# Kernel tuning notes

Measured on AMD Instinct MI355X. Metric: run time of the kernel, lower is better.

The kernel has to match this reference:

```python
import jax, jax.numpy as jnp
import numpy as np

B, C, S = 256, 1024, 14   # batch, channels, spatial (frozen by y.view(b,c,14,14))
C2 = 15                   # channels2 in the module
CAT = C // 2 * 3 + C2     # 1551 = 15 + 512 + 1024
EPS = 1e-5


def _conv(x, w, b, groups, pad):
    out = jax.lax.conv_general_dilated(
        x, w, window_strides=(1, 1), padding=((pad, pad), (pad, pad)),
        dimension_numbers=('NCHW', 'OIHW', 'NCHW'), feature_group_count=groups)
    return out + b[None, :, None, None]


def _bn(x, gamma, beta):
    # training-mode BatchNorm2d: biased batch stats over (N,H,W)
    m = x.mean((0, 2, 3), keepdims=True)
    v = x.var((0, 2, 3), keepdims=True)
    return (x - m) * jax.lax.rsqrt(v + EPS) * gamma[None, :, None, None] + beta[None, :, None, None]


def setup_inputs() -> dict:
    key = jax.random.key(0)
    ks = jax.random.split(key, 16)
    r = C2 // 7  # = 2
    inp = {
        'y': jax.random.normal(ks[0], (B, C2, S * S), jnp.float32),
        'x': jax.random.normal(ks[1], (B, C, S, S), jnp.float32),
        'fc1_w': jax.random.normal(ks[2], (r, C2), jnp.float32) * 0.2,
        'fc2_w': jax.random.normal(ks[3], (C2, r), jnp.float32) * 0.2,
        'conv_w': jax.random.normal(ks[4], (C // 2, C, 1, 1), jnp.float32) * 0.03,
        'conv_b': jnp.zeros((C // 2,), jnp.float32),
        'dconv_w': jax.random.normal(ks[5], (C, 1, 3, 3), jnp.float32) * 0.2,
        'dconv_b': jnp.zeros((C,), jnp.float32),
        'dw1_w': jax.random.normal(ks[6], (CAT, 1, 3, 3), jnp.float32) * 0.2,
        'dw1_b': jnp.zeros((CAT,), jnp.float32),
        'pw1_w': jax.random.normal(ks[7], (C // 2, CAT, 1, 1), jnp.float32) * 0.03,
        'pw1_b': jnp.zeros((C // 2,), jnp.float32),
        'gamma': jnp.ones((C // 2,), jnp.float32),
        'beta': jnp.zeros((C // 2,), jnp.float32),
        'n': 0,
    }
    return inp


def reference(y, x, fc1_w, fc2_w, conv_w, conv_b, dconv_w, dconv_b,
              dw1_w, dw1_b, pw1_w, pw1_b, gamma, beta, n):
    b = y.shape[0]
    y4 = y.reshape(b, C2, S, S)
    # SE block on the 15 sub-channels
    g = y4.mean((2, 3))                              # (b, 15) global avg pool
    h = jax.nn.relu(g @ fc1_w.T) @ fc2_w.T           # (b, 15)
    y1 = y4 * jax.nn.sigmoid(h)[:, :, None, None]
    # depthwise conv on x, then per-(b,c) row covariance of the 14x14 map
    x1 = _conv(x, dconv_w, dconv_b, C, 1)            # (b, C, 14, 14)
    x2 = jax.lax.stop_gradient(x1)                   # .detach() in the original
    xc = x2 - x2.mean(-1, keepdims=True)             # np.cov: rows=vars, cols=obs
    cov = jnp.einsum('bcik,bcjk->bcij', xc, xc) / (S - 1)
    z = _conv(cov, conv_w, conv_b, 1, 0)             # 1x1 conv C -> C//2
    z = jax.nn.sigmoid(_bn(z, gamma, beta))
    for _ in range(n):                               # n=0 at these shapes
        y1 = jax.image.resize(y1, (y1.shape[0], y1.shape[1], y1.shape[2] * 2, y1.shape[3] * 2), 'bilinear')
    cat = jnp.concatenate([y1, z, x], axis=1)        # (b, 1551, 14, 14)
    o = _conv(cat, dw1_w, dw1_b, CAT, 1)             # depthwise 3x3
    o = _conv(o, pw1_w, pw1_b, 1, 0)                 # pointwise 1x1 -> C//2
    return jax.nn.relu(_bn(o, gamma, beta))
```

## Files before the change

### kernel.cpp

```cpp
#include <hip/hip_runtime.h>

typedef unsigned int u32;
typedef unsigned short u16;
typedef __attribute__((ext_vector_type(8))) short bf16x8;
typedef __attribute__((ext_vector_type(4))) float f32x4;
typedef __attribute__((ext_vector_type(4))) u32 u32x4;

#define EPSBN 1e-5f

#define GLDS16(gp, lp) __builtin_amdgcn_global_load_lds( \
    (const __attribute__((address_space(1))) u32*)(gp), \
    (__attribute__((address_space(3))) u32*)(lp), 16, 0, 0)

#define OFF_ADW    0ull
#define OFF_COVT   0ull
#define OFF_S      160563200ull
#define OFF_WBZ    160578560ull
#define OFF_WBP    161627136ull
#define OFF_STATSZ 163265536ull
#define OFF_STATSO 163269632ull
#define OFF_SCZ    163273728ull
#define OFF_SHZ    163275776ull
#define OFF_SCO    163277824ull
#define OFF_SHO    163279872ull

static __device__ __forceinline__ float bf2f(u16 h){
  u32 u = ((u32)h) << 16; float f; __builtin_memcpy(&f, &u, 4); return f;
}
static __device__ __forceinline__ u16 f2bf(float f){
  u32 u; __builtin_memcpy(&u, &f, 4);
  u = (u + 0x7fffu + ((u >> 16) & 1u)) >> 16;
  return (u16)u;
}

__global__ __launch_bounds__(64) void se_kernel(const float* __restrict__ y,
    const float* __restrict__ fc1, const float* __restrict__ fc2, float* __restrict__ sse){
  __shared__ float g[15];
  __shared__ float t[2];
  int b = blockIdx.x, l = threadIdx.x;
  for (int c = 0; c < 15; ++c){
    float p = 0.f;
    for (int k = l; k < 196; k += 64) p += y[((size_t)b*15 + c)*196 + k];
    p += __shfl_xor(p, 32); p += __shfl_xor(p, 16); p += __shfl_xor(p, 8);
    p += __shfl_xor(p, 4);  p += __shfl_xor(p, 2);  p += __shfl_xor(p, 1);
    if (l == 0) g[c] = p * (1.f/196.f);
  }
  __syncthreads();
  if (l < 2){
    float a = 0.f;
    for (int c = 0; c < 15; ++c) a += g[c] * fc1[l*15 + c];
    t[l] = fmaxf(a, 0.f);
  }
  __syncthreads();
  if (l < 15){
    float h = t[0]*fc2[l*2] + t[1]*fc2[l*2+1];
    sse[b*15 + l] = 1.f / (1.f + __expf(-h));
  }
}

__global__ void wconv_kernel(const float* __restrict__ cw, const float* __restrict__ pw,
                             u16* __restrict__ wbz, u16* __restrict__ wbp){
  u32 stride = gridDim.x * blockDim.x;
  for (u32 i = blockIdx.x*blockDim.x + threadIdx.x; i < 524288u; i += stride)
    wbz[i] = f2bf(cw[i]);
  for (u32 i = blockIdx.x*blockDim.x + threadIdx.x; i < 819200u; i += stride){
    u32 n = i / 1600u, k = i - n*1600u;
    wbp[i] = f2bf(k < 1551u ? pw[(size_t)n*1551 + k] : 0.f);
  }
}

__global__ __launch_bounds__(256,5) void cov_kernel(const float* __restrict__ x,
    const float* __restrict__ dcw, const float* __restrict__ dcb, u16* __restrict__ covT){
  __shared__ __align__(16) float xs[16*200];
  __shared__ __align__(16) u32 xcb[16*132];
  __shared__ float wls[16][9];
  __shared__ float wlb[16];
  u32* covL32 = (u32*)xs;

  int tid = threadIdx.x;
  int c0 = blockIdx.x * 16, b = blockIdx.y;

  {
    const float4* xg = (const float4*)(x + ((size_t)b*1024 + c0)*196);
    for (int i = tid; i < 784; i += 256){
      float4 v = xg[i];
      u32 c = (u32)i / 49u, p4 = (u32)i - c*49u;
      *(float4*)&xs[c*200u + p4*4u] = v;
    }
  }
  if (tid < 144) wls[tid/9][tid%9] = dcw[(size_t)(c0 + tid/9)*9 + (tid%9)];
  if (tid < 16) wlb[tid] = dcb[c0 + tid];
  __syncthreads();

  {
    int c = tid >> 4, i = tid & 15;
    u32 q[8];
    #pragma unroll
    for (int j = 0; j < 8; ++j) q[j] = 0u;
    if (i < 14){
      float wr[9];
      #pragma unroll
      for (int qq = 0; qq < 9; ++qq) wr[qq] = wls[c][qq];
      float topm = (i > 0) ? 1.f : 0.f, botm = (i < 13) ? 1.f : 0.f;
      wr[0] *= topm; wr[1] *= topm; wr[2] *= topm;
      wr[6] *= botm; wr[7] *= botm; wr[8] *= botm;
      float bb = wlb[c];
      float rr[3][16];
      #pragma unroll
      for (int d = 0; d < 3; ++d){
        rr[d][0] = 0.f; rr[d][15] = 0.f;
        int rowr = i + d - 1;
        rowr = rowr < 0 ? 0 : (rowr > 13 ? 13 : rowr);
        const float* src = &xs[c*200 + rowr*14];
        #pragma unroll
        for (int j = 0; j < 7; ++j)
          *(float2*)&rr[d][1 + 2*j] = *(const float2*)&src[2*j];
      }
      float ov[14];
      #pragma unroll
      for (int k = 0; k < 14; ++k){
        float a = bb;
        #pragma unroll
        for (int dy = 0; dy < 3; ++dy)
          #pragma unroll
          for (int dx = 0; dx < 3; ++dx)
            a += wr[dy*3+dx] * rr[dy][k + dx];
        ov[k] = a;
      }
      float mean = 0.f;
      #pragma unroll
      for (int k = 0; k < 14; ++k) mean += ov[k];
      mean *= (1.f/14.f);
      #pragma unroll
      for (int j = 0; j < 7; ++j){
        u32 lo = f2bf(ov[2*j]   - mean);
        u32 hi = f2bf(ov[2*j+1] - mean);
        q[j] = lo | (hi << 16);
      }
    }
    u32x4 q0 = {q[0], q[1], q[2], q[3]};
    u32x4 q1 = {q[4], q[5], q[6], q[7]};
    *(u32x4*)&xcb[c*132 + i*8]     = q0;
    *(u32x4*)&xcb[c*132 + i*8 + 4] = q1;
  }
  __syncthreads();

  {
    int w = tid >> 6, l = tid & 63, lr = l & 15, lq = l >> 4;
    #pragma unroll
    for (int pp = 0; pp < 2; ++pp){
      int clo = w*4 + 2*pp;
      bf16x8 alo = {0,0,0,0,0,0,0,0}, ahi = {0,0,0,0,0,0,0,0};
      if (lq < 2){
        alo = *(const bf16x8*)&xcb[clo*132 + lr*8 + lq*4];
        ahi = *(const bf16x8*)&xcb[(clo+1)*132 + lr*8 + lq*4];
      }
      f32x4 dlo = {0.f,0.f,0.f,0.f}, dhi = {0.f,0.f,0.f,0.f};
      dlo = __builtin_amdgcn_mfma_f32_16x16x32_bf16(alo, alo, dlo, 0, 0, 0);
      dhi = __builtin_amdgcn_mfma_f32_16x16x32_bf16(ahi, ahi, dhi, 0, 0, 0);
      if (lr < 14){
        int cp = w*2 + pp;
        #pragma unroll
        for (int r = 0; r < 4; ++r){
          int rowi = lq*4 + r;
          if (rowi < 14){
            u32 vv = (u32)f2bf(dlo[r] * (1.f/13.f)) | ((u32)f2bf(dhi[r] * (1.f/13.f)) << 16);
            covL32[cp*210 + rowi*14 + lr] = vv;
          }
        }
      }
    }
  }
  __syncthreads();

  for (int i = tid; i < 1568; i += 256){
    int cp = i & 7, ij = i >> 3;
    u32 v = covL32[cp*210 + ij];
    *(u32*)(covT + ((size_t)(b*196 + ij)*1024 + c0 + 2*cp)) = v;
  }
}

__global__ __launch_bounds__(256,5) void adw_kernel(
    const float* __restrict__ y, const float* __restrict__ sse,
    const u16* __restrict__ zT, const float* __restrict__ scz, const float* __restrict__ shz,
    const float* __restrict__ x, const float* __restrict__ dw1w, const float* __restrict__ dw1b,
    u16* __restrict__ Adw){
  __shared__ __align__(16) float ms[32*202];
  __shared__ float wd[32][9];
  __shared__ float bd[32];
  int tid = threadIdx.x;
  int cc0 = blockIdx.x * 32, b = blockIdx.y;

  for (int i = tid; i < 288; i += 256){
    int c = i / 9, q = i - c*9;
    int cc = cc0 + c;
    wd[c][q] = (cc < 1551) ? dw1w[(size_t)cc*9 + q] : 0.f;
  }
  if (tid < 32) bd[tid] = (cc0 + tid < 1551) ? dw1b[cc0 + tid] : 0.f;

  if (cc0 < 15){
    int ny = 15;
    for (int i = tid; i < ny*196; i += 256){
      u32 c = (u32)i / 196u, p = (u32)i - c*196u;
      ms[c*202u + p] = y[((size_t)b*15 + c)*196 + p] * sse[b*15 + c];
    }
  }
  {
    int zs = cc0 > 15 ? cc0 : 15;
    int ze = cc0 + 32 < 527 ? cc0 + 32 : 527;
    if (zs < ze){
      int nz = ze - zs, lbase = zs - cc0, obase = zs - 15;
      const u16* zrow = zT + (size_t)obase*50176 + (size_t)b*196;
      for (int i = tid; i < nz*98; i += 256){
        u32 oo = (u32)i / 98u, pp = (u32)i - oo*98u;
        u32 v = *(const u32*)(zrow + (size_t)oo*50176 + pp*2u);
        int o = obase + (int)oo;
        float s = scz[o], h = shz[o];
        float v0 = bf2f((u16)(v & 0xffffu)) * s + h;
        float v1 = bf2f((u16)(v >> 16))     * s + h;
        v0 = 1.f / (1.f + __expf(-v0));
        v1 = 1.f / (1.f + __expf(-v1));
        float2 fv = {v0, v1};
        *(float2*)&ms[(u32)(lbase + (int)oo)*202u + pp*2u] = fv;
      }
    }
  }
  {
    int xs_ = cc0 > 527 ? cc0 : 527;
    int xe = cc0 + 32 < 1551 ? cc0 + 32 : 1551;
    if (xs_ < xe){
      int nx = xe - xs_, lbase = xs_ - cc0, cxs = xs_ - 527;
      const float4* xg = (const float4*)(x + ((size_t)b*1024 + cxs)*196);
      for (int i = tid; i < nx*49; i += 256){
        float4 v = xg[i];
        u32 c = (u32)i / 49u, p4 = (u32)i - c*49u;
        float* dst = &ms[(u32)(lbase + (int)c)*202u + p4*4u];
        float2 lo = {v.x, v.y}, hi = {v.z, v.w};
        *(float2*)dst = lo;
        *(float2*)(dst + 2) = hi;
      }
    }
  }
  {
    int ps = cc0 > 1551 ? cc0 : 1551;
    int pe = cc0 + 32;
    if (ps < pe){
      int np = pe - ps, lbase = ps - cc0;
      for (int i = tid; i < np*196; i += 256){
        u32 c = (u32)i / 196u, p = (u32)i - c*196u;
        ms[(u32)(lbase + (int)c)*202u + p] = 0.f;
      }
    }
  }
  __syncthreads();

  for (int t = tid; t < 448; t += 256){
    int cc = t & 31, i = t >> 5;
    float wr[9];
    #pragma unroll
    for (int qq = 0; qq < 9; ++qq) wr[qq] = wd[cc][qq];
    float topm = (i > 0) ? 1.f : 0.f, botm = (i < 13) ? 1.f : 0.f;
    wr[0] *= topm; wr[1] *= topm; wr[2] *= topm;
    wr[6] *= botm; wr[7] *= botm; wr[8] *= botm;
    float bb = bd[cc];
    float rr[3][16];
    #pragma unroll
    for (int d = 0; d < 3; ++d){
      rr[d][0] = 0.f; rr[d][15] = 0.f;
      int rowr = i + d - 1;
      rowr = rowr < 0 ? 0 : (rowr > 13 ? 13 : rowr);
      const float* src = &ms[cc*202 + rowr*14];
      #pragma unroll
      for (int j = 0; j < 7; ++j)
        *(float2*)&rr[d][1 + 2*j] = *(const float2*)&src[2*j];
    }
    size_t obase = ((size_t)b*196 + i*14) * 1600 + cc0 + cc;
    #pragma unroll
    for (int k = 0; k < 14; ++k){
      float a = bb;
      #pragma unroll
      for (int dy = 0; dy < 3; ++dy)
        #pragma unroll
        for (int dx = 0; dx < 3; ++dx)
          a += wr[dy*3+dx] * rr[dy][k + dx];
      Adw[obase + (size_t)k*1600] = f2bf(a);
    }
  }
}

template<int MODE>
__global__ __launch_bounds__(256,3) void gemm_kernel(
    const u16* __restrict__ A, const u16* __restrict__ Bw,
    const float* __restrict__ bias, void* __restrict__ outp,
    float* __restrict__ stats, int K){
  __shared__ __align__(16) char smem[33280];
  u16* As = (u16*)smem;
  u16* Bs = (u16*)(smem + 16384);

  int tid = threadIdx.x;
  int w = tid >> 6, l = tid & 63;
  int wm = w >> 1, wn = w & 1;
  int lr = l & 15, lq = l >> 4;
  int m0 = blockIdx.y * 128;
  int n0 = blockIdx.x * 128;

  f32x4 acc[4][4] = {};
  int kTiles = K >> 6;

  for (int kt = 0; kt < kTiles; ++kt){
    if (kt) __syncthreads();
    #pragma unroll
    for (int i = 0; i < 4; ++i){
      int s = tid + i*256;
      int row = s >> 3, c8 = s & 7, sc = c8 ^ (row & 7);
      GLDS16(A  + (size_t)(m0 + row)*K + kt*64 + sc*8, As + s*8);
      GLDS16(Bw + (size_t)(n0 + row)*K + kt*64 + sc*8, Bs + s*8);
    }
    __syncthreads();
    #pragma unroll
    for (int ks = 0; ks < 2; ++ks){
      bf16x8 af[4], bfv[4];
      #pragma unroll
      for (int mi = 0; mi < 4; ++mi){
        int row = wm*64 + mi*16 + lr;
        int q = (ks*4 + lq) ^ (row & 7);
        af[mi] = *(const bf16x8*)(As + row*64 + q*8);
      }
      #pragma unroll
      for (int ni = 0; ni < 4; ++ni){
        int row = wn*64 + ni*16 + lr;
        int q = (ks*4 + lq) ^ (row & 7);
        bfv[ni] = *(const bf16x8*)(Bs + row*64 + q*8);
      }
      #pragma unroll
      for (int mi = 0; mi < 4; ++mi)
        #pragma unroll
        for (int ni = 0; ni < 4; ++ni)
          acc[mi][ni] = __builtin_amdgcn_mfma_f32_16x16x32_bf16(af[mi], bfv[ni], acc[mi][ni], 0, 0, 0);
    }
  }

  #pragma unroll
  for (int ni = 0; ni < 4; ++ni){
    int col = n0 + wn*64 + ni*16 + lr;
    float bb = bias[col];
    float s1 = 0.f, s2 = 0.f;
    #pragma unroll
    for (int mi = 0; mi < 4; ++mi)
      #pragma unroll
      for (int r = 0; r < 4; ++r){
        float v = acc[mi][ni][r] + bb;
        acc[mi][ni][r] = v;
        s1 += v; s2 += v*v;
      }
    s1 += __shfl_xor(s1, 16); s1 += __shfl_xor(s1, 32);
    s2 += __shfl_xor(s2, 16); s2 += __shfl_xor(s2, 32);
    if (lq == 0){
      atomicAdd(&stats[col], s1);
      atomicAdd(&stats[512 + col], s2);
    }
  }

  __syncthreads();
  float* eb = (float*)smem;
  #pragma unroll
  for (int rnd = 0; rnd < 2; ++rnd){
    if (wm == rnd){
      float* e = eb + wn * (64*65);
      #pragma unroll
      for (int mi = 0; mi < 4; ++mi)
        #pragma unroll
        for (int ni = 0; ni < 4; ++ni)
          #pragma unroll
          for (int r = 0; r < 4; ++r)
            e[(mi*16 + lq*4 + r)*65 + ni*16 + lr] = acc[mi][ni][r];
      int m = m0 + wm*64 + l;
      if (MODE == 0){
        u16* ob = (u16*)outp + (size_t)(n0 + wn*64)*50176 + m;
        #pragma unroll 8
        for (int no = 0; no < 64; ++no)
          ob[(size_t)no*50176] = f2bf(e[l*65 + no]);
      } else {
        u32 bq = (u32)m / 196u;
        u32 ij = (u32)m - bq*196u;
        float* ob = (float*)outp + ((size_t)bq*512 + n0 + wn*64)*196 + ij;
        #pragma unroll 8
        for (int no = 0; no < 64; ++no)
          ob[(size_t)no*196] = e[l*65 + no];
      }
    }
    __syncthreads();
  }
}

__global__ void bnprep_kernel(const float* __restrict__ stats, const float* __restrict__ gamma,
    const float* __restrict__ beta, float* __restrict__ sc, float* __restrict__ sh){
  int o = threadIdx.x;
  float m = stats[o] * (1.f/50176.f);
  float v = stats[512+o] * (1.f/50176.f) - m*m;
  float inv = rsqrtf(v + EPSBN);
  float g = gamma[o] * inv;
  sc[o] = g;
  sh[o] = beta[o] - m*g;
}

__global__ void final_kernel(float4* __restrict__ o4, const float* __restrict__ sc,
                             const float* __restrict__ sh){
  u32 stride = gridDim.x * blockDim.x;
  for (u32 i = blockIdx.x*blockDim.x + threadIdx.x; i < 6422528u; i += stride){
    u32 oc = (i / 49u) & 511u;
    float s = sc[oc], t = sh[oc];
    float4 v = o4[i];
    v.x = fmaxf(fmaf(v.x, s, t), 0.f);
    v.y = fmaxf(fmaf(v.y, s, t), 0.f);
    v.z = fmaxf(fmaf(v.z, s, t), 0.f);
    v.w = fmaxf(fmaf(v.w, s, t), 0.f);
    o4[i] = v;
  }
}

extern "C" void kernel_launch(void* const* d_in, const int* in_sizes, int n_in,
                              void* d_out, int out_size, void* d_ws, size_t ws_size,
                              hipStream_t stream){
  (void)in_sizes; (void)n_in; (void)out_size; (void)ws_size;
  const float* y      = (const float*)d_in[0];
  const float* x      = (const float*)d_in[1];
  const float* fc1    = (const float*)d_in[2];
  const float* fc2    = (const float*)d_in[3];
  const float* convw  = (const float*)d_in[4];
  const float* convb  = (const float*)d_in[5];
  const float* dconvw = (const float*)d_in[6];
  const float* dconvb = (const float*)d_in[7];
  const float* dw1w   = (const float*)d_in[8];
  const float* dw1b   = (const float*)d_in[9];
  const float* pw1w   = (const float*)d_in[10];
  const float* pw1b   = (const float*)d_in[11];
  const float* gamma  = (const float*)d_in[12];
  const float* beta   = (const float*)d_in[13];

  char* ws = (char*)d_ws;
  u16* covT   = (u16*)(ws + OFF_COVT);
  u16* Adw    = (u16*)(ws + OFF_ADW);
  float* sse  = (float*)(ws + OFF_S);
  u16* wbz    = (u16*)(ws + OFF_WBZ);
  u16* wbp    = (u16*)(ws + OFF_WBP);
  float* statsZ = (float*)(ws + OFF_STATSZ);
  float* statsO = (float*)(ws + OFF_STATSO);
  float* scz  = (float*)(ws + OFF_SCZ);
  float* shz  = (float*)(ws + OFF_SHZ);
  float* sco  = (float*)(ws + OFF_SCO);
  float* sho  = (float*)(ws + OFF_SHO);
  u16* zT     = (u16*)d_out;
  float* outf = (float*)d_out;

  hipMemsetAsync(statsZ, 0, 8192, stream);
  se_kernel<<<256, 64, 0, stream>>>(y, fc1, fc2, sse);
  wconv_kernel<<<2048, 256, 0, stream>>>(convw, pw1w, wbz, wbp);
  cov_kernel<<<dim3(64, 256), 256, 0, stream>>>(x, dconvw, dconvb, covT);
  gemm_kernel<0><<<dim3(4, 392), 256, 0, stream>>>(covT, wbz, convb, (void*)zT, statsZ, 1024);
  bnprep_kernel<<<1, 512, 0, stream>>>(statsZ, gamma, beta, scz, shz);
  adw_kernel<<<dim3(50, 256), 256, 0, stream>>>(y, sse, zT, scz, shz, x, dw1w, dw1b, Adw);
  gemm_kernel<1><<<dim3(4, 392), 256, 0, stream>>>(Adw, wbp, pw1b, (void*)outf, statsO, 1600);
  bnprep_kernel<<<1, 512, 0, stream>>>(statsO, gamma, beta, sco, sho);
  final_kernel<<<8192, 256, 0, stream>>>((float4*)outf, sco, sho);
}
```

Baseline: 524.3 us.

## Retile GEMMs so each 512-thread block covers all 512 output columns

Both pointwise GEMMs now run one 512-thread block per 64-row M tile, and that block computes all 512 N columns across 8 waves. The large activation matrix A is therefore read from global memory only once, not once per 128-column N tile. In exchange, every block reloads the full 512x64 weight slab into LDS on each k step. That raises LDS use to 72 KB and limits how many blocks fit per CU. There is still no double buffering to hide load latency.

```diff
diff --git a/kernel.cpp b/kernel.cpp
--- a/kernel.cpp
+++ b/kernel.cpp
@@ -289,32 +289,34 @@
 }
 
 template<int MODE>
-__global__ __launch_bounds__(256,3) void gemm_kernel(
+__global__ __launch_bounds__(512,4) void gemm_kernel(
     const u16* __restrict__ A, const u16* __restrict__ Bw,
     const float* __restrict__ bias, void* __restrict__ outp,
     float* __restrict__ stats, int K){
-  __shared__ __align__(16) char smem[33280];
+  __shared__ __align__(16) char smem[73728];
   u16* As = (u16*)smem;
-  u16* Bs = (u16*)(smem + 16384);
+  u16* Bs = (u16*)(smem + 8192);
 
   int tid = threadIdx.x;
   int w = tid >> 6, l = tid & 63;
-  int wm = w >> 1, wn = w & 1;
   int lr = l & 15, lq = l >> 4;
-  int m0 = blockIdx.y * 128;
-  int n0 = blockIdx.x * 128;
+  int m0 = blockIdx.x * 64;
 
   f32x4 acc[4][4] = {};
   int kTiles = K >> 6;
 
   for (int kt = 0; kt < kTiles; ++kt){
     if (kt) __syncthreads();
-    #pragma unroll
-    for (int i = 0; i < 4; ++i){
-      int s = tid + i*256;
+    {
+      int s = tid;
       int row = s >> 3, c8 = s & 7, sc = c8 ^ (row & 7);
-      GLDS16(A  + (size_t)(m0 + row)*K + kt*64 + sc*8, As + s*8);
-      GLDS16(Bw + (size_t)(n0 + row)*K + kt*64 + sc*8, Bs + s*8);
+      GLDS16(A + (size_t)(m0 + row)*K + kt*64 + sc*8, As + s*8);
+    }
+    #pragma unroll
+    for (int i = 0; i < 8; ++i){
+      int s = tid + i*512;
+      int row = s >> 3, c8 = s & 7, sc = c8 ^ (row & 7);
+      GLDS16(Bw + (size_t)row*K + kt*64 + sc*8, Bs + s*8);
     }
     __syncthreads();
     #pragma unroll
@@ -322,13 +324,13 @@
       bf16x8 af[4], bfv[4];
       #pragma unroll
       for (int mi = 0; mi < 4; ++mi){
-        int row = wm*64 + mi*16 + lr;
+        int row = mi*16 + lr;
         int q = (ks*4 + lq) ^ (row & 7);
         af[mi] = *(const bf16x8*)(As + row*64 + q*8);
       }
       #pragma unroll
       for (int ni = 0; ni < 4; ++ni){
-        int row = wn*64 + ni*16 + lr;
+        int row = w*64 + ni*16 + lr;
         int q = (ks*4 + lq) ^ (row & 7);
         bfv[ni] = *(const bf16x8*)(Bs + row*64 + q*8);
       }
@@ -342,7 +344,7 @@
 
   #pragma unroll
   for (int ni = 0; ni < 4; ++ni){
-    int col = n0 + wn*64 + ni*16 + lr;
+    int col = w*64 + ni*16 + lr;
     float bb = bias[col];
     float s1 = 0.f, s2 = 0.f;
     #pragma unroll
@@ -365,8 +367,8 @@
   float* eb = (float*)smem;
   #pragma unroll
   for (int rnd = 0; rnd < 2; ++rnd){
-    if (wm == rnd){
-      float* e = eb + wn * (64*65);
+    if ((w >> 2) == rnd){
+      float* e = eb + (w & 3) * (64*65);
       #pragma unroll
       for (int mi = 0; mi < 4; ++mi)
         #pragma unroll
@@ -374,16 +376,16 @@
           #pragma unroll
           for (int r = 0; r < 4; ++r)
             e[(mi*16 + lq*4 + r)*65 + ni*16 + lr] = acc[mi][ni][r];
-      int m = m0 + wm*64 + l;
+      int m = m0 + l;
       if (MODE == 0){
-        u16* ob = (u16*)outp + (size_t)(n0 + wn*64)*50176 + m;
+        u16* ob = (u16*)outp + (size_t)(w*64)*50176 + m;
         #pragma unroll 8
         for (int no = 0; no < 64; ++no)
           ob[(size_t)no*50176] = f2bf(e[l*65 + no]);
       } else {
         u32 bq = (u32)m / 196u;
         u32 ij = (u32)m - bq*196u;
-        float* ob = (float*)outp + ((size_t)bq*512 + n0 + wn*64)*196 + ij;
+        float* ob = (float*)outp + ((size_t)bq*512 + w*64)*196 + ij;
         #pragma unroll 8
         for (int no = 0; no < 64; ++no)
           ob[(size_t)no*196] = e[l*65 + no];
@@ -457,10 +459,10 @@
   se_kernel<<<256, 64, 0, stream>>>(y, fc1, fc2, sse);
   wconv_kernel<<<2048, 256, 0, stream>>>(convw, pw1w, wbz, wbp);
   cov_kernel<<<dim3(64, 256), 256, 0, stream>>>(x, dconvw, dconvb, covT);
-  gemm_kernel<0><<<dim3(4, 392), 256, 0, stream>>>(covT, wbz, convb, (void*)zT, statsZ, 1024);
+  gemm_kernel<0><<<784, 512, 0, stream>>>(covT, wbz, convb, (void*)zT, statsZ, 1024);
   bnprep_kernel<<<1, 512, 0, stream>>>(statsZ, gamma, beta, scz, shz);
   adw_kernel<<<dim3(50, 256), 256, 0, stream>>>(y, sse, zT, scz, shz, x, dw1w, dw1b, Adw);
-  gemm_kernel<1><<<dim3(4, 392), 256, 0, stream>>>(Adw, wbp, pw1b, (void*)outf, statsO, 1600);
+  gemm_kernel<1><<<784, 512, 0, stream>>>(Adw, wbp, pw1b, (void*)outf, statsO, 1600);
   bnprep_kernel<<<1, 512, 0, stream>>>(statsO, gamma, beta, sco, sho);
   final_kernel<<<8192, 256, 0, stream>>>((float4*)outf, sco, sho);
 }
```

Result: slower. 558.8 us (+6.6%).
